# Kernel tuning notes

Measured on AMD Instinct MI355X. Metric: run time of the kernel, lower is better.

Reference implementation:

```python
import jax, jax.numpy as jnp
import numpy as np

B, D, O, E, H, K = 4096, 1024, 1024, 8, 4096, 2


def setup_inputs() -> dict:
    key = jax.random.key(0)
    ks = jax.random.split(key, 5)
    scale_g = 1.0 / np.sqrt(D)
    scale_1 = 1.0 / np.sqrt(D)
    scale_2 = 1.0 / np.sqrt(H)
    return {
        "x": jax.random.normal(ks[0], (B, D), jnp.float32),
        "gate_w": jax.random.normal(ks[1], (D, E), jnp.float32) * scale_g,
        "gate_b": jnp.zeros((E,), jnp.float32),
        "w1": jax.random.normal(ks[2], (E, D, H), jnp.float32) * scale_1,
        "b1": jnp.zeros((E, H), jnp.float32),
        "w2": jax.random.normal(ks[3], (E, H, O), jnp.float32) * scale_2,
        "b2": jnp.zeros((E, O), jnp.float32),
    }


def reference(x, gate_w, gate_b, w1, b1, w2, b2):
    # Router: top-k logits, softmax over the k selected logits only
    logits = x @ gate_w + gate_b                      # [B, E]
    top_vals, top_idx = jax.lax.top_k(logits, K)      # [B, K]
    routing_w = jax.nn.softmax(top_vals, axis=-1)     # [B, K]

    # Dense all-expert MLP (grouped GEMM), then gather the k selected outputs
    h = jax.nn.relu(jnp.einsum("bd,edh->beh", x, w1) + b1)  # [B, E, H]
    y = jnp.einsum("beh,eho->beo", h, w2) + b2              # [B, E, O]
    sel = jnp.take_along_axis(y, top_idx[:, :, None], axis=1)  # [B, K, O]
    return jnp.sum(routing_w[:, :, None] * sel, axis=1)        # [B, O]
```

## Files before the change

kernel.cpp:

```cpp
#include <hip/hip_runtime.h>
#include <stdint.h>

typedef short bf16x8 __attribute__((ext_vector_type(8)));
typedef float f32x4  __attribute__((ext_vector_type(4)));

constexpr int BT = 4096;
constexpr int DD = 1024;
constexpr int OO = 1024;
constexpr int EE = 8;
constexpr int HH = 4096;
constexpr int SLOTS = 2 * BT;

constexpr int BM = 256, BN = 256, BK = 32;
constexpr int RING = 4;
constexpr int A_USH = BM * BK;
constexpr int SLOT_USH = (BM + BN) * BK;
constexpr int MAXT = 40;

__device__ __forceinline__ unsigned short f2bf(float f) {
  unsigned u = __float_as_uint(f);
  u += 0x7fffu + ((u >> 16) & 1u);
  return (unsigned short)(u >> 16);
}

__device__ __forceinline__ void glds16(const unsigned short* g, unsigned short* l) {
  __builtin_amdgcn_global_load_lds(
      (const __attribute__((address_space(1))) void*)g,
      (__attribute__((address_space(3))) void*)l, 16, 0, 0);
}

__global__ __launch_bounds__(256) void router_k(const float* __restrict__ x,
                                                const float* __restrict__ gw,
                                                const float* __restrict__ gb,
                                                unsigned short* __restrict__ xb,
                                                int* __restrict__ cnt,
                                                int* __restrict__ list,
                                                float* __restrict__ rw) {
  int wave = threadIdx.x >> 6, lane = threadIdx.x & 63;
  int b = blockIdx.x * 4 + wave;
  const float* xrow = x + (size_t)b * DD;
  float acc[8];
#pragma unroll
  for (int e = 0; e < 8; ++e) acc[e] = 0.f;
#pragma unroll
  for (int i = 0; i < 4; ++i) {
    int d0 = i * 256 + lane * 4;
    float4 v = *(const float4*)&xrow[d0];
    unsigned lo = (unsigned)f2bf(v.x) | ((unsigned)f2bf(v.y) << 16);
    unsigned hi = (unsigned)f2bf(v.z) | ((unsigned)f2bf(v.w) << 16);
    *(uint2*)&xb[(size_t)b * DD + d0] = make_uint2(lo, hi);
    const float* g0 = &gw[(size_t)d0 * 8];
    float fv[4] = {v.x, v.y, v.z, v.w};
#pragma unroll
    for (int q = 0; q < 4; ++q) {
      float4 ga = *(const float4*)&g0[q * 8];
      float4 gc = *(const float4*)&g0[q * 8 + 4];
      acc[0] += fv[q] * ga.x; acc[1] += fv[q] * ga.y;
      acc[2] += fv[q] * ga.z; acc[3] += fv[q] * ga.w;
      acc[4] += fv[q] * gc.x; acc[5] += fv[q] * gc.y;
      acc[6] += fv[q] * gc.z; acc[7] += fv[q] * gc.w;
    }
  }
#pragma unroll
  for (int off = 32; off > 0; off >>= 1) {
#pragma unroll
    for (int e = 0; e < 8; ++e) acc[e] += __shfl_down(acc[e], off);
  }
  if (lane == 0) {
    float v[8];
#pragma unroll
    for (int e = 0; e < 8; ++e) v[e] = acc[e] + gb[e];
    int i0 = 0;
#pragma unroll
    for (int e = 1; e < 8; ++e) if (v[e] > v[i0]) i0 = e;
    int i1 = (i0 == 0) ? 1 : 0;
#pragma unroll
    for (int e = 0; e < 8; ++e) if (e != i0 && v[e] > v[i1]) i1 = e;
    float e1 = __expf(v[i1] - v[i0]);
    float inv = 1.0f / (1.0f + e1);
    int p0 = atomicAdd(&cnt[i0], 1);
    list[i0 * BT + p0] = 2 * b;     rw[2 * b]     = inv;
    int p1 = atomicAdd(&cnt[i1], 1);
    list[i1 * BT + p1] = 2 * b + 1; rw[2 * b + 1] = e1 * inv;
  }
}

__global__ void tilemap_k(const int* __restrict__ cnt, int* __restrict__ tmap,
                          int* __restrict__ ntiles) {
  if (threadIdx.x == 0 && blockIdx.x == 0) {
    int t = 0, basewalk = 0;
    for (int e = 0; e < EE; ++e) {
      int c = cnt[e];
      for (int m0 = 0; m0 < c; m0 += BM) {
        tmap[4 * t] = e; tmap[4 * t + 1] = m0; tmap[4 * t + 2] = basewalk + m0; ++t;
      }
      basewalk += c;
    }
    *ntiles = t;
  }
}

__global__ __launch_bounds__(256) void cvt_t_k(const float* __restrict__ src,
                                               unsigned short* __restrict__ dst,
                                               int R, int C) {
  __shared__ unsigned short tile[64][66];
  int e = blockIdx.z;
  const float* s = src + (size_t)e * R * C;
  unsigned short* d = dst + (size_t)e * R * C;
  int r0 = blockIdx.x << 6, c0 = blockIdx.y << 6;
  int t = threadIdx.x;
#pragma unroll
  for (int p = 0; p < 4; ++p) {
    int ch = p * 256 + t;
    int rr = ch >> 4, cc = (ch & 15) << 2;
    float4 v = *(const float4*)&s[(size_t)(r0 + rr) * C + c0 + cc];
    unsigned lo = (unsigned)f2bf(v.x) | ((unsigned)f2bf(v.y) << 16);
    unsigned hi = (unsigned)f2bf(v.z) | ((unsigned)f2bf(v.w) << 16);
    *(uint2*)&tile[rr][cc] = make_uint2(lo, hi);
  }
  __syncthreads();
#pragma unroll
  for (int p = 0; p < 4; ++p) {
    int ch = p * 256 + t;
    int cc = ch >> 4, rr = (ch & 15) << 2;
    unsigned short v0 = tile[rr + 0][cc];
    unsigned short v1 = tile[rr + 1][cc];
    unsigned short v2 = tile[rr + 2][cc];
    unsigned short v3 = tile[rr + 3][cc];
    unsigned lo = (unsigned)v0 | ((unsigned)v1 << 16);
    unsigned hi = (unsigned)v2 | ((unsigned)v3 << 16);
    *(uint2*)&d[(size_t)(c0 + cc) * R + r0 + rr] = make_uint2(lo, hi);
  }
}

__global__ __launch_bounds__(512, 2) void gemm1_k(const unsigned short* __restrict__ xb,
                                                  const unsigned short* __restrict__ w1t,
                                                  const float* __restrict__ b1,
                                                  const int* __restrict__ cnt,
                                                  const int* __restrict__ list,
                                                  const int* __restrict__ tmap,
                                                  const int* __restrict__ ntiles,
                                                  unsigned short* __restrict__ hc) {
  int ti = blockIdx.y;
  if (ti >= *ntiles) return;
  int e = tmap[4 * ti], m0 = tmap[4 * ti + 1], base = tmap[4 * ti + 2];
  int cnt_e = cnt[e];
  int n0 = blockIdx.x * BN;

  __shared__ int slotbuf[BM];
  __shared__ __align__(16) unsigned short lds[RING * SLOT_USH];

  int t = threadIdx.x;
  if (t < BM) {
    int r = m0 + t;
    slotbuf[t] = list[e * BT + (r < cnt_e ? r : 0)];
  }
  __syncthreads();

  int w = t >> 6, l = t & 63, lm = l & 15, lq = l >> 4;
  int wr = w >> 2, wc = w & 3;

  const unsigned short* aS[2];
  const unsigned short* bS[2];
  int dA[2], dB[2];
#pragma unroll
  for (int j = 0; j < 2; ++j) {
    int row = j * 128 + w * 16 + (l >> 2);
    int sch = ((l & 3) ^ ((row >> 1) & 3)) * 8;
    aS[j] = xb + (size_t)(slotbuf[row] >> 1) * DD + sch;
    bS[j] = w1t + (size_t)e * HH * DD + (size_t)(n0 + row) * DD + sch;
    dA[j] = j * 4096 + w * 512;
    dB[j] = A_USH + j * 4096 + w * 512;
  }

  int xc = lq ^ ((lm >> 1) & 3);
  int afo[8], bfo[4];
#pragma unroll
  for (int mi = 0; mi < 8; ++mi) afo[mi] = (wr * 128 + mi * 16 + lm) * BK + xc * 8;
#pragma unroll
  for (int ni = 0; ni < 4; ++ni) bfo[ni] = A_USH + (wc * 64 + ni * 16 + lm) * BK + xc * 8;

  f32x4 acc[8][4];
#pragma unroll
  for (int mi = 0; mi < 8; ++mi)
#pragma unroll
    for (int ni = 0; ni < 4; ++ni) acc[mi][ni] = f32x4{0.f, 0.f, 0.f, 0.f};

  constexpr int NT = DD / BK;

#pragma unroll
  for (int p = 0; p < RING - 1; ++p) {
    unsigned short* Lb = lds + p * SLOT_USH;
    glds16(aS[0] + p * BK, Lb + dA[0]);
    glds16(aS[1] + p * BK, Lb + dA[1]);
    glds16(bS[0] + p * BK, Lb + dB[0]);
    glds16(bS[1] + p * BK, Lb + dB[1]);
  }
  asm volatile("s_waitcnt vmcnt(8)" ::: "memory");
  __builtin_amdgcn_s_barrier();
  asm volatile("" ::: "memory");

  for (int tt = 0; tt < NT; ++tt) {
    {
      int ts = tt + 3;
      int ko = (ts < NT ? ts : NT - 1) * BK;
      unsigned short* Lb = lds + (ts & 3) * SLOT_USH;
      glds16(aS[0] + ko, Lb + dA[0]);
      glds16(aS[1] + ko, Lb + dA[1]);
      glds16(bS[0] + ko, Lb + dB[0]);
      glds16(bS[1] + ko, Lb + dB[1]);
    }
    const unsigned short* Lc = lds + (tt & 3) * SLOT_USH;
    bf16x8 af[8], bf[4];
#pragma unroll
    for (int mi = 0; mi < 8; ++mi) af[mi] = *(const bf16x8*)&Lc[afo[mi]];
#pragma unroll
    for (int ni = 0; ni < 4; ++ni) bf[ni] = *(const bf16x8*)&Lc[bfo[ni]];
    __builtin_amdgcn_s_setprio(1);
#pragma unroll
    for (int mi = 0; mi < 8; ++mi)
#pragma unroll
      for (int ni = 0; ni < 4; ++ni)
        acc[mi][ni] = __builtin_amdgcn_mfma_f32_16x16x32_bf16(af[mi], bf[ni], acc[mi][ni], 0, 0, 0);
    __builtin_amdgcn_s_setprio(0);
    asm volatile("s_waitcnt vmcnt(8)" ::: "memory");
    __builtin_amdgcn_s_barrier();
    asm volatile("" ::: "memory");
  }

  asm volatile("s_waitcnt vmcnt(0)" ::: "memory");
  __builtin_amdgcn_s_barrier();
  asm volatile("" ::: "memory");
  unsigned short* cb = lds + w * 8192;
  float bias[4];
#pragma unroll
  for (int ni = 0; ni < 4; ++ni) bias[ni] = b1[e * HH + n0 + wc * 64 + ni * 16 + lm];
#pragma unroll
  for (int mi = 0; mi < 8; ++mi)
#pragma unroll
    for (int ni = 0; ni < 4; ++ni)
#pragma unroll
      for (int r = 0; r < 4; ++r)
        cb[(mi * 16 + lq * 4 + r) * 64 + ni * 16 + lm] =
            f2bf(fmaxf(acc[mi][ni][r] + bias[ni], 0.0f));
  asm volatile("s_waitcnt lgkmcnt(0)" ::: "memory");
#pragma unroll
  for (int it = 0; it < 16; ++it) {
    int rr = it * 8 + (l >> 3), chk = l & 7;
    int grow = wr * 128 + rr;
    if (m0 + grow < cnt_e) {
      uint4 v = *(const uint4*)&cb[rr * 64 + chk * 8];
      *(uint4*)&hc[(size_t)(base + grow) * HH + n0 + wc * 64 + chk * 8] = v;
    }
  }
}

__global__ __launch_bounds__(512, 2) void gemm2_k(const unsigned short* __restrict__ hc,
                                                  const unsigned short* __restrict__ w2t,
                                                  const float* __restrict__ b2,
                                                  const int* __restrict__ cnt,
                                                  const int* __restrict__ list,
                                                  const int* __restrict__ tmap,
                                                  const int* __restrict__ ntiles,
                                                  const float* __restrict__ rw,
                                                  float* __restrict__ ybuf,
                                                  float* __restrict__ out) {
  int ti = blockIdx.y;
  if (ti >= *ntiles) return;
  int e = tmap[4 * ti], m0 = tmap[4 * ti + 1], base = tmap[4 * ti + 2];
  int cnt_e = cnt[e];
  int n0 = blockIdx.x * BN;
  int z = blockIdx.z;
  int ksl = HH / gridDim.z;
  int kb0 = z * ksl;
  int NT = ksl / BK;

  __shared__ int slotbuf[BM];
  __shared__ float rwbuf[BM];
  __shared__ __align__(16) unsigned short lds[RING * SLOT_USH];

  int t = threadIdx.x;
  if (t < BM) {
    int r = m0 + t;
    int s_ = list[e * BT + (r < cnt_e ? r : 0)];
    slotbuf[t] = s_;
    rwbuf[t] = rw[s_];
  }
  __syncthreads();

  int w = t >> 6, l = t & 63, lm = l & 15, lq = l >> 4;
  int wr = w >> 2, wc = w & 3;

  const unsigned short* aS[2];
  const unsigned short* bS[2];
  int dA[2], dB[2];
#pragma unroll
  for (int j = 0; j < 2; ++j) {
    int row = j * 128 + w * 16 + (l >> 2);
    int sch = ((l & 3) ^ ((row >> 1) & 3)) * 8;
    int gr = base + row; if (gr > SLOTS - 1) gr = SLOTS - 1;
    aS[j] = hc + (size_t)gr * HH + kb0 + sch;
    bS[j] = w2t + (size_t)e * OO * HH + (size_t)(n0 + row) * HH + kb0 + sch;
    dA[j] = j * 4096 + w * 512;
    dB[j] = A_USH + j * 4096 + w * 512;
  }

  int xc = lq ^ ((lm >> 1) & 3);
  int afo[8], bfo[4];
#pragma unroll
  for (int mi = 0; mi < 8; ++mi) afo[mi] = (wr * 128 + mi * 16 + lm) * BK + xc * 8;
#pragma unroll
  for (int ni = 0; ni < 4; ++ni) bfo[ni] = A_USH + (wc * 64 + ni * 16 + lm) * BK + xc * 8;

  f32x4 acc[8][4];
#pragma unroll
  for (int mi = 0; mi < 8; ++mi)
#pragma unroll
    for (int ni = 0; ni < 4; ++ni) acc[mi][ni] = f32x4{0.f, 0.f, 0.f, 0.f};

#pragma unroll
  for (int p = 0; p < RING - 1; ++p) {
    unsigned short* Lb = lds + p * SLOT_USH;
    glds16(aS[0] + p * BK, Lb + dA[0]);
    glds16(aS[1] + p * BK, Lb + dA[1]);
    glds16(bS[0] + p * BK, Lb + dB[0]);
    glds16(bS[1] + p * BK, Lb + dB[1]);
  }
  asm volatile("s_waitcnt vmcnt(8)" ::: "memory");
  __builtin_amdgcn_s_barrier();
  asm volatile("" ::: "memory");

  for (int tt = 0; tt < NT; ++tt) {
    {
      int ts = tt + 3;
      int ko = (ts < NT ? ts : NT - 1) * BK;
      unsigned short* Lb = lds + (ts & 3) * SLOT_USH;
      glds16(aS[0] + ko, Lb + dA[0]);
      glds16(aS[1] + ko, Lb + dA[1]);
      glds16(bS[0] + ko, Lb + dB[0]);
      glds16(bS[1] + ko, Lb + dB[1]);
    }
    const unsigned short* Lc = lds + (tt & 3) * SLOT_USH;
    bf16x8 af[8], bf[4];
#pragma unroll
    for (int mi = 0; mi < 8; ++mi) af[mi] = *(const bf16x8*)&Lc[afo[mi]];
#pragma unroll
    for (int ni = 0; ni < 4; ++ni) bf[ni] = *(const bf16x8*)&Lc[bfo[ni]];
    __builtin_amdgcn_s_setprio(1);
#pragma unroll
    for (int mi = 0; mi < 8; ++mi)
#pragma unroll
      for (int ni = 0; ni < 4; ++ni)
        acc[mi][ni] = __builtin_amdgcn_mfma_f32_16x16x32_bf16(af[mi], bf[ni], acc[mi][ni], 0, 0, 0);
    __builtin_amdgcn_s_setprio(0);
    asm volatile("s_waitcnt vmcnt(8)" ::: "memory");
    __builtin_amdgcn_s_barrier();
    asm volatile("" ::: "memory");
  }
  asm volatile("s_waitcnt vmcnt(0)" ::: "memory");

  bool addb = (z == 0);
  size_t ybase = (size_t)z * SLOTS;
#pragma unroll
  for (int ni = 0; ni < 4; ++ni) {
    int ncol = n0 + wc * 64 + ni * 16 + lm;
    float bias = addb ? b2[e * OO + ncol] : 0.0f;
#pragma unroll
    for (int mi = 0; mi < 8; ++mi)
#pragma unroll
      for (int r = 0; r < 4; ++r) {
        int lrow = wr * 128 + mi * 16 + lq * 4 + r;
        if (m0 + lrow < cnt_e) {
          float v = (acc[mi][ni][r] + bias) * rwbuf[lrow];
          int slot = slotbuf[lrow];
          if (ybuf) ybuf[(ybase + slot) * OO + ncol] = v;
          else      atomicAdd(&out[(size_t)(slot >> 1) * OO + ncol], v);
        }
      }
  }
}

__global__ __launch_bounds__(256) void combine_k(const float* __restrict__ y,
                                                 float* __restrict__ out, int nz) {
  int i = blockIdx.x * 256 + threadIdx.x;
  int b = i >> 8, c = i & 255;
  f32x4 acc = {0.f, 0.f, 0.f, 0.f};
  for (int z = 0; z < nz; ++z) {
#pragma unroll
    for (int k = 0; k < 2; ++k) {
      const float4 v = *(const float4*)&y[((size_t)z * SLOTS + 2 * b + k) * OO + c * 4];
      acc[0] += v.x; acc[1] += v.y; acc[2] += v.z; acc[3] += v.w;
    }
  }
  *(f32x4*)&out[(size_t)b * OO + c * 4] = acc;
}

extern "C" void kernel_launch(void* const* d_in, const int* in_sizes, int n_in,
                              void* d_out, int out_size, void* d_ws, size_t ws_size,
                              hipStream_t stream) {
  const float* x  = (const float*)d_in[0];
  const float* gw = (const float*)d_in[1];
  const float* gb = (const float*)d_in[2];
  const float* w1 = (const float*)d_in[3];
  const float* b1 = (const float*)d_in[4];
  const float* w2 = (const float*)d_in[5];
  const float* b2 = (const float*)d_in[6];
  float* out = (float*)d_out;
  char* ws = (char*)d_ws;

  int*            cnt    = (int*)(ws);
  int*            ntiles = (int*)(ws + 64);
  int*            tmap   = (int*)(ws + 128);
  float*          rw     = (float*)(ws + 4096);
  int*            list   = (int*)(ws + (64u << 10));
  unsigned short* xb     = (unsigned short*)(ws + (1u  << 20));
  unsigned short* wt     = (unsigned short*)(ws + (9u  << 20));
  unsigned short* hc     = (unsigned short*)(ws + (73u << 20));
  float*          ybuf   = (float*)(ws + (138u << 20));

  size_t need_min = (138u << 20);
  if (ws_size < need_min) return;
  int zsplit;
  float* ypass;
  if (ws_size >= (138u << 20) + (size_t)2 * SLOTS * OO * 4) { zsplit = 2; ypass = ybuf; }
  else if (ws_size >= (138u << 20) + (size_t)SLOTS * OO * 4) { zsplit = 1; ypass = ybuf; }
  else { zsplit = 2; ypass = nullptr; }

  hipMemsetAsync(cnt, 0, 64, stream);
  if (!ypass) hipMemsetAsync(out, 0, (size_t)BT * OO * sizeof(float), stream);

  router_k<<<BT / 4, 256, 0, stream>>>(x, gw, gb, xb, cnt, list, rw);
  tilemap_k<<<1, 64, 0, stream>>>(cnt, tmap, ntiles);
  cvt_t_k<<<dim3(DD / 64, HH / 64, EE), 256, 0, stream>>>(w1, wt, DD, HH);
  gemm1_k<<<dim3(HH / BN, MAXT), 512, 0, stream>>>(xb, wt, b1, cnt, list, tmap, ntiles, hc);
  cvt_t_k<<<dim3(HH / 64, OO / 64, EE), 256, 0, stream>>>(w2, wt, HH, OO);
  gemm2_k<<<dim3(OO / BN, MAXT, zsplit), 512, 0, stream>>>(hc, wt, b2, cnt, list, tmap, ntiles, rw, ypass, out);
  if (ypass)
    combine_k<<<BT * OO / 1024, 256, 0, stream>>>(ybuf, out, zsplit);
}
```

Before: 733.8 us.

## Shrink GEMM tiles to 128x128 and fuse weight conversion into router and GEMM1 launches

Both grouped GEMMs drop from 256x256 tiles with 512 threads and a 4-deep ring to 128x128 tiles with 256 threads, a 3-deep ring and 3 blocks per CU. MAXT rises to match the finer row tiling. The w1 transpose-convert is folded into the router launch as extra blocks, and when the workspace is large enough the w2 convert runs as extra blocks alongside GEMM1, writing to a separate buffer so the two can overlap. The aim is to cut launch count, fill CUs better with more, smaller blocks, and hide conversion work behind compute, at the cost of less operand reuse per tile and more redundant A/B traffic.

```diff
diff --git a/kernel.cpp b/kernel.cpp
--- a/kernel.cpp
+++ b/kernel.cpp
@@ -11,11 +11,11 @@
 constexpr int HH = 4096;
 constexpr int SLOTS = 2 * BT;
 
-constexpr int BM = 256, BN = 256, BK = 32;
-constexpr int RING = 4;
+constexpr int BM = 128, BN = 128, BK = 32;
 constexpr int A_USH = BM * BK;
 constexpr int SLOT_USH = (BM + BN) * BK;
-constexpr int MAXT = 40;
+constexpr int MAXT = 72;
+constexpr int G1_BLKS = 32 * MAXT;
 
 __device__ __forceinline__ unsigned short f2bf(float f) {
   unsigned u = __float_as_uint(f);
@@ -29,15 +29,56 @@
       (__attribute__((address_space(3))) void*)l, 16, 0, 0);
 }
 
-__global__ __launch_bounds__(256) void router_k(const float* __restrict__ x,
+__device__ __forceinline__ void cvt_body(const float* __restrict__ src,
+                                         unsigned short* __restrict__ dst,
+                                         int R, int C, int e, int r0, int c0, int t,
+                                         unsigned short (*tile)[66]) {
+  const float* s = src + (size_t)e * R * C;
+  unsigned short* d = dst + (size_t)e * R * C;
+#pragma unroll
+  for (int p = 0; p < 4; ++p) {
+    int ch = p * 256 + t;
+    int rr = ch >> 4, cc = (ch & 15) << 2;
+    float4 v = *(const float4*)&s[(size_t)(r0 + rr) * C + c0 + cc];
+    unsigned lo = (unsigned)f2bf(v.x) | ((unsigned)f2bf(v.y) << 16);
+    unsigned hi = (unsigned)f2bf(v.z) | ((unsigned)f2bf(v.w) << 16);
+    *(uint2*)&tile[rr][cc] = make_uint2(lo, hi);
+  }
+  __syncthreads();
+#pragma unroll
+  for (int p = 0; p < 4; ++p) {
+    int ch = p * 256 + t;
+    int cc = ch >> 4, rr = (ch & 15) << 2;
+    unsigned short v0 = tile[rr + 0][cc];
+    unsigned short v1 = tile[rr + 1][cc];
+    unsigned short v2 = tile[rr + 2][cc];
+    unsigned short v3 = tile[rr + 3][cc];
+    unsigned lo = (unsigned)v0 | ((unsigned)v1 << 16);
+    unsigned hi = (unsigned)v2 | ((unsigned)v3 << 16);
+    *(uint2*)&d[(size_t)(c0 + cc) * R + r0 + rr] = make_uint2(lo, hi);
+  }
+}
+
+__global__ __launch_bounds__(256) void fusedA_k(const float* __restrict__ x,
                                                 const float* __restrict__ gw,
                                                 const float* __restrict__ gb,
+                                                const float* __restrict__ w1,
                                                 unsigned short* __restrict__ xb,
                                                 int* __restrict__ cnt,
                                                 int* __restrict__ list,
-                                                float* __restrict__ rw) {
+                                                float* __restrict__ rw,
+                                                unsigned short* __restrict__ w1t) {
+  __shared__ unsigned short tile[64][66];
+  int bid = blockIdx.x;
+  if (bid >= 1024) {
+    int idx = bid - 1024;
+    int e = idx >> 10, rem = idx & 1023;
+    int r0 = (rem & 15) << 6, c0 = (rem >> 4) << 6;
+    cvt_body(w1, w1t, DD, HH, e, r0, c0, threadIdx.x, tile);
+    return;
+  }
   int wave = threadIdx.x >> 6, lane = threadIdx.x & 63;
-  int b = blockIdx.x * 4 + wave;
+  int b = bid * 4 + wave;
   const float* xrow = x + (size_t)b * DD;
   float acc[8];
 #pragma unroll
@@ -104,51 +145,36 @@
                                                unsigned short* __restrict__ dst,
                                                int R, int C) {
   __shared__ unsigned short tile[64][66];
-  int e = blockIdx.z;
-  const float* s = src + (size_t)e * R * C;
-  unsigned short* d = dst + (size_t)e * R * C;
-  int r0 = blockIdx.x << 6, c0 = blockIdx.y << 6;
-  int t = threadIdx.x;
-#pragma unroll
-  for (int p = 0; p < 4; ++p) {
-    int ch = p * 256 + t;
-    int rr = ch >> 4, cc = (ch & 15) << 2;
-    float4 v = *(const float4*)&s[(size_t)(r0 + rr) * C + c0 + cc];
-    unsigned lo = (unsigned)f2bf(v.x) | ((unsigned)f2bf(v.y) << 16);
-    unsigned hi = (unsigned)f2bf(v.z) | ((unsigned)f2bf(v.w) << 16);
-    *(uint2*)&tile[rr][cc] = make_uint2(lo, hi);
-  }
-  __syncthreads();
-#pragma unroll
-  for (int p = 0; p < 4; ++p) {
-    int ch = p * 256 + t;
-    int cc = ch >> 4, rr = (ch & 15) << 2;
-    unsigned short v0 = tile[rr + 0][cc];
-    unsigned short v1 = tile[rr + 1][cc];
-    unsigned short v2 = tile[rr + 2][cc];
-    unsigned short v3 = tile[rr + 3][cc];
-    unsigned lo = (unsigned)v0 | ((unsigned)v1 << 16);
-    unsigned hi = (unsigned)v2 | ((unsigned)v3 << 16);
-    *(uint2*)&d[(size_t)(c0 + cc) * R + r0 + rr] = make_uint2(lo, hi);
-  }
-}
-
-__global__ __launch_bounds__(512, 2) void gemm1_k(const unsigned short* __restrict__ xb,
-                                                  const unsigned short* __restrict__ w1t,
-                                                  const float* __restrict__ b1,
-                                                  const int* __restrict__ cnt,
-                                                  const int* __restrict__ list,
-                                                  const int* __restrict__ tmap,
-                                                  const int* __restrict__ ntiles,
-                                                  unsigned short* __restrict__ hc) {
-  int ti = blockIdx.y;
+  cvt_body(src, dst, R, C, blockIdx.z, blockIdx.x << 6, blockIdx.y << 6,
+           threadIdx.x, tile);
+}
+
+__global__ __launch_bounds__(256, 3) void fusedB_k(const unsigned short* __restrict__ xb,
+                                                   const unsigned short* __restrict__ w1t,
+                                                   const float* __restrict__ b1,
+                                                   const int* __restrict__ cnt,
+                                                   const int* __restrict__ list,
+                                                   const int* __restrict__ tmap,
+                                                   const int* __restrict__ ntiles,
+                                                   unsigned short* __restrict__ hc,
+                                                   const float* __restrict__ w2,
+                                                   unsigned short* __restrict__ w2t) {
+  __shared__ __align__(16) unsigned short lds[3 * SLOT_USH];
+  __shared__ int slotbuf[BM];
+  int bid = blockIdx.x;
+  if (bid >= G1_BLKS) {
+    int idx = bid - G1_BLKS;
+    int e = idx >> 10, rem = idx & 1023;
+    int r0 = (rem & 63) << 6, c0 = (rem >> 6) << 6;
+    cvt_body(w2, w2t, HH, OO, e, r0, c0, threadIdx.x,
+             (unsigned short (*)[66])lds);
+    return;
+  }
+  int ti = bid >> 5;
   if (ti >= *ntiles) return;
   int e = tmap[4 * ti], m0 = tmap[4 * ti + 1], base = tmap[4 * ti + 2];
   int cnt_e = cnt[e];
-  int n0 = blockIdx.x * BN;
-
-  __shared__ int slotbuf[BM];
-  __shared__ __align__(16) unsigned short lds[RING * SLOT_USH];
+  int n0 = (bid & 31) * BN;
 
   int t = threadIdx.x;
   if (t < BM) {
@@ -158,85 +184,88 @@
   __syncthreads();
 
   int w = t >> 6, l = t & 63, lm = l & 15, lq = l >> 4;
-  int wr = w >> 2, wc = w & 3;
+  int wm = (w >> 1) * 64, wn = (w & 1) * 64;
 
   const unsigned short* aS[2];
   const unsigned short* bS[2];
   int dA[2], dB[2];
 #pragma unroll
   for (int j = 0; j < 2; ++j) {
-    int row = j * 128 + w * 16 + (l >> 2);
+    int row = w * 32 + j * 16 + (l >> 2);
     int sch = ((l & 3) ^ ((row >> 1) & 3)) * 8;
     aS[j] = xb + (size_t)(slotbuf[row] >> 1) * DD + sch;
     bS[j] = w1t + (size_t)e * HH * DD + (size_t)(n0 + row) * DD + sch;
-    dA[j] = j * 4096 + w * 512;
-    dB[j] = A_USH + j * 4096 + w * 512;
-  }
-
-  int xc = lq ^ ((lm >> 1) & 3);
-  int afo[8], bfo[4];
-#pragma unroll
-  for (int mi = 0; mi < 8; ++mi) afo[mi] = (wr * 128 + mi * 16 + lm) * BK + xc * 8;
-#pragma unroll
-  for (int ni = 0; ni < 4; ++ni) bfo[ni] = A_USH + (wc * 64 + ni * 16 + lm) * BK + xc * 8;
-
-  f32x4 acc[8][4];
-#pragma unroll
-  for (int mi = 0; mi < 8; ++mi)
+    dA[j] = w * 1024 + j * 512;
+    dB[j] = A_USH + w * 1024 + j * 512;
+  }
+
+  int xs = (lq ^ ((lm >> 1) & 3)) * 8;
+  int afo[4], bfo[4];
+#pragma unroll
+  for (int mi = 0; mi < 4; ++mi) afo[mi] = (wm + mi * 16 + lm) * BK + xs;
+#pragma unroll
+  for (int ni = 0; ni < 4; ++ni) bfo[ni] = A_USH + (wn + ni * 16 + lm) * BK + xs;
+
+  f32x4 acc[4][4];
+#pragma unroll
+  for (int mi = 0; mi < 4; ++mi)
 #pragma unroll
     for (int ni = 0; ni < 4; ++ni) acc[mi][ni] = f32x4{0.f, 0.f, 0.f, 0.f};
 
   constexpr int NT = DD / BK;
 
 #pragma unroll
-  for (int p = 0; p < RING - 1; ++p) {
+  for (int p = 0; p < 2; ++p) {
     unsigned short* Lb = lds + p * SLOT_USH;
     glds16(aS[0] + p * BK, Lb + dA[0]);
     glds16(aS[1] + p * BK, Lb + dA[1]);
     glds16(bS[0] + p * BK, Lb + dB[0]);
     glds16(bS[1] + p * BK, Lb + dB[1]);
   }
-  asm volatile("s_waitcnt vmcnt(8)" ::: "memory");
+  asm volatile("s_waitcnt vmcnt(4)" ::: "memory");
   __builtin_amdgcn_s_barrier();
   asm volatile("" ::: "memory");
 
+  int sc = 0, ss = 2;
   for (int tt = 0; tt < NT; ++tt) {
     {
-      int ts = tt + 3;
+      int ts = tt + 2;
       int ko = (ts < NT ? ts : NT - 1) * BK;
-      unsigned short* Lb = lds + (ts & 3) * SLOT_USH;
+      unsigned short* Lb = lds + ss * SLOT_USH;
       glds16(aS[0] + ko, Lb + dA[0]);
       glds16(aS[1] + ko, Lb + dA[1]);
       glds16(bS[0] + ko, Lb + dB[0]);
       glds16(bS[1] + ko, Lb + dB[1]);
     }
-    const unsigned short* Lc = lds + (tt & 3) * SLOT_USH;
-    bf16x8 af[8], bf[4];
-#pragma unroll
-    for (int mi = 0; mi < 8; ++mi) af[mi] = *(const bf16x8*)&Lc[afo[mi]];
+    const unsigned short* Lc = lds + sc * SLOT_USH;
+    bf16x8 af[4], bf[4];
+#pragma unroll
+    for (int mi = 0; mi < 4; ++mi) af[mi] = *(const bf16x8*)&Lc[afo[mi]];
 #pragma unroll
     for (int ni = 0; ni < 4; ++ni) bf[ni] = *(const bf16x8*)&Lc[bfo[ni]];
     __builtin_amdgcn_s_setprio(1);
 #pragma unroll
-    for (int mi = 0; mi < 8; ++mi)
+    for (int mi = 0; mi < 4; ++mi)
 #pragma unroll
       for (int ni = 0; ni < 4; ++ni)
         acc[mi][ni] = __builtin_amdgcn_mfma_f32_16x16x32_bf16(af[mi], bf[ni], acc[mi][ni], 0, 0, 0);
     __builtin_amdgcn_s_setprio(0);
-    asm volatile("s_waitcnt vmcnt(8)" ::: "memory");
+    asm volatile("s_waitcnt vmcnt(4)" ::: "memory");
     __builtin_amdgcn_s_barrier();
     asm volatile("" ::: "memory");
+    if (++sc == 3) sc = 0;
+    if (++ss == 3) ss = 0;
   }
 
   asm volatile("s_waitcnt vmcnt(0)" ::: "memory");
   __builtin_amdgcn_s_barrier();
   asm volatile("" ::: "memory");
-  unsigned short* cb = lds + w * 8192;
+  unsigned short* cb = lds + w * 4096;
   float bias[4];
 #pragma unroll
-  for (int ni = 0; ni < 4; ++ni) bias[ni] = b1[e * HH + n0 + wc * 64 + ni * 16 + lm];
-#pragma unroll
-  for (int mi = 0; mi < 8; ++mi)
+  for (int ni = 0; ni < 4; ++ni) bias[ni] = b1[e * HH + n0 + wn + ni * 16 + lm];
+#pragma unroll
+  for (int mi = 0; mi < 4; ++mi)
 #pragma unroll
     for (int ni = 0; ni < 4; ++ni)
 #pragma unroll
@@ -245,17 +274,17 @@
             f2bf(fmaxf(acc[mi][ni][r] + bias[ni], 0.0f));
   asm volatile("s_waitcnt lgkmcnt(0)" ::: "memory");
 #pragma unroll
-  for (int it = 0; it < 16; ++it) {
+  for (int it = 0; it < 8; ++it) {
     int rr = it * 8 + (l >> 3), chk = l & 7;
-    int grow = wr * 128 + rr;
+    int grow = wm + rr;
     if (m0 + grow < cnt_e) {
       uint4 v = *(const uint4*)&cb[rr * 64 + chk * 8];
-      *(uint4*)&hc[(size_t)(base + grow) * HH + n0 + wc * 64 + chk * 8] = v;
-    }
-  }
-}
-
-__global__ __launch_bounds__(512, 2) void gemm2_k(const unsigned short* __restrict__ hc,
+      *(uint4*)&hc[(size_t)(base + grow) * HH + n0 + wn + chk * 8] = v;
+    }
+  }
+}
+
+__global__ __launch_bounds__(256, 3) void gemm2_k(const unsigned short* __restrict__ hc,
                                                   const unsigned short* __restrict__ w2t,
                                                   const float* __restrict__ b2,
                                                   const int* __restrict__ cnt,
@@ -271,13 +300,12 @@
   int cnt_e = cnt[e];
   int n0 = blockIdx.x * BN;
   int z = blockIdx.z;
-  int ksl = HH / gridDim.z;
-  int kb0 = z * ksl;
-  int NT = ksl / BK;
-
+  int kb0 = z * (HH / 2);
+  constexpr int NT = (HH / 2) / BK;
+
+  __shared__ __align__(16) unsigned short lds[3 * SLOT_USH];
   __shared__ int slotbuf[BM];
   __shared__ float rwbuf[BM];
-  __shared__ __align__(16) unsigned short lds[RING * SLOT_USH];
 
   int t = threadIdx.x;
   if (t < BM) {
@@ -289,73 +317,76 @@
   __syncthreads();
 
   int w = t >> 6, l = t & 63, lm = l & 15, lq = l >> 4;
-  int wr = w >> 2, wc = w & 3;
+  int wm = (w >> 1) * 64, wn = (w & 1) * 64;
 
   const unsigned short* aS[2];
   const unsigned short* bS[2];
   int dA[2], dB[2];
 #pragma unroll
   for (int j = 0; j < 2; ++j) {
-    int row = j * 128 + w * 16 + (l >> 2);
+    int row = w * 32 + j * 16 + (l >> 2);
     int sch = ((l & 3) ^ ((row >> 1) & 3)) * 8;
     int gr = base + row; if (gr > SLOTS - 1) gr = SLOTS - 1;
     aS[j] = hc + (size_t)gr * HH + kb0 + sch;
     bS[j] = w2t + (size_t)e * OO * HH + (size_t)(n0 + row) * HH + kb0 + sch;
-    dA[j] = j * 4096 + w * 512;
-    dB[j] = A_USH + j * 4096 + w * 512;
-  }
-
-  int xc = lq ^ ((lm >> 1) & 3);
-  int afo[8], bfo[4];
-#pragma unroll
-  for (int mi = 0; mi < 8; ++mi) afo[mi] = (wr * 128 + mi * 16 + lm) * BK + xc * 8;
-#pragma unroll
-  for (int ni = 0; ni < 4; ++ni) bfo[ni] = A_USH + (wc * 64 + ni * 16 + lm) * BK + xc * 8;
-
-  f32x4 acc[8][4];
-#pragma unroll
-  for (int mi = 0; mi < 8; ++mi)
+    dA[j] = w * 1024 + j * 512;
+    dB[j] = A_USH + w * 1024 + j * 512;
+  }
+
+  int xs = (lq ^ ((lm >> 1) & 3)) * 8;
+  int afo[4], bfo[4];
+#pragma unroll
+  for (int mi = 0; mi < 4; ++mi) afo[mi] = (wm + mi * 16 + lm) * BK + xs;
+#pragma unroll
+  for (int ni = 0; ni < 4; ++ni) bfo[ni] = A_USH + (wn + ni * 16 + lm) * BK + xs;
+
+  f32x4 acc[4][4];
+#pragma unroll
+  for (int mi = 0; mi < 4; ++mi)
 #pragma unroll
     for (int ni = 0; ni < 4; ++ni) acc[mi][ni] = f32x4{0.f, 0.f, 0.f, 0.f};
 
 #pragma unroll
-  for (int p = 0; p < RING - 1; ++p) {
+  for (int p = 0; p < 2; ++p) {
     unsigned short* Lb = lds + p * SLOT_USH;
     glds16(aS[0] + p * BK, Lb + dA[0]);
     glds16(aS[1] + p * BK, Lb + dA[1]);
     glds16(bS[0] + p * BK, Lb + dB[0]);
     glds16(bS[1] + p * BK, Lb + dB[1]);
   }
-  asm volatile("s_waitcnt vmcnt(8)" ::: "memory");
+  asm volatile("s_waitcnt vmcnt(4)" ::: "memory");
   __builtin_amdgcn_s_barrier();
   asm volatile("" ::: "memory");
 
+  int sc = 0, ss = 2;
   for (int tt = 0; tt < NT; ++tt) {
     {
-      int ts = tt + 3;
+      int ts = tt + 2;
       int ko = (ts < NT ? ts : NT - 1) * BK;
-      unsigned short* Lb = lds + (ts & 3) * SLOT_USH;
+      unsigned short* Lb = lds + ss * SLOT_USH;
       glds16(aS[0] + ko, Lb + dA[0]);
       glds16(aS[1] + ko, Lb + dA[1]);
       glds16(bS[0] + ko, Lb + dB[0]);
       glds16(bS[1] + ko, Lb + dB[1]);
     }
-    const unsigned short* Lc = lds + (tt & 3) * SLOT_USH;
-    bf16x8 af[8], bf[4];
-#pragma unroll
-    for (int mi = 0; mi < 8; ++mi) af[mi] = *(const bf16x8*)&Lc[afo[mi]];
+    const unsigned short* Lc = lds + sc * SLOT_USH;
+    bf16x8 af[4], bf[4];
+#pragma unroll
+    for (int mi = 0; mi < 4; ++mi) af[mi] = *(const bf16x8*)&Lc[afo[mi]];
 #pragma unroll
     for (int ni = 0; ni < 4; ++ni) bf[ni] = *(const bf16x8*)&Lc[bfo[ni]];
     __builtin_amdgcn_s_setprio(1);
 #pragma unroll
-    for (int mi = 0; mi < 8; ++mi)
+    for (int mi = 0; mi < 4; ++mi)
 #pragma unroll
       for (int ni = 0; ni < 4; ++ni)
         acc[mi][ni] = __builtin_amdgcn_mfma_f32_16x16x32_bf16(af[mi], bf[ni], acc[mi][ni], 0, 0, 0);
     __builtin_amdgcn_s_setprio(0);
-    asm volatile("s_waitcnt vmcnt(8)" ::: "memory");
+    asm volatile("s_waitcnt vmcnt(4)" ::: "memory");
     __builtin_amdgcn_s_barrier();
     asm volatile("" ::: "memory");
+    if (++sc == 3) sc = 0;
+    if (++ss == 3) ss = 0;
   }
   asm volatile("s_waitcnt vmcnt(0)" ::: "memory");
 
@@ -363,13 +394,13 @@
   size_t ybase = (size_t)z * SLOTS;
 #pragma unroll
   for (int ni = 0; ni < 4; ++ni) {
-    int ncol = n0 + wc * 64 + ni * 16 + lm;
+    int ncol = n0 + wn + ni * 16 + lm;
     float bias = addb ? b2[e * OO + ncol] : 0.0f;
 #pragma unroll
-    for (int mi = 0; mi < 8; ++mi)
+    for (int mi = 0; mi < 4; ++mi)
 #pragma unroll
       for (int r = 0; r < 4; ++r) {
-        int lrow = wr * 128 + mi * 16 + lq * 4 + r;
+        int lrow = wm + mi * 16 + lq * 4 + r;
         if (m0 + lrow < cnt_e) {
           float v = (acc[mi][ni][r] + bias) * rwbuf[lrow];
           int slot = slotbuf[lrow];
@@ -414,27 +445,34 @@
   float*          rw     = (float*)(ws + 4096);
   int*            list   = (int*)(ws + (64u << 10));
   unsigned short* xb     = (unsigned short*)(ws + (1u  << 20));
-  unsigned short* wt     = (unsigned short*)(ws + (9u  << 20));
-  unsigned short* hc     = (unsigned short*)(ws + (73u << 20));
-  float*          ybuf   = (float*)(ws + (138u << 20));
-
-  size_t need_min = (138u << 20);
-  if (ws_size < need_min) return;
-  int zsplit;
-  float* ypass;
-  if (ws_size >= (138u << 20) + (size_t)2 * SLOTS * OO * 4) { zsplit = 2; ypass = ybuf; }
-  else if (ws_size >= (138u << 20) + (size_t)SLOTS * OO * 4) { zsplit = 1; ypass = ybuf; }
-  else { zsplit = 2; ypass = nullptr; }
-
+  unsigned short* w1t    = (unsigned short*)(ws + (9u  << 20));
+
+  bool roomy = ws_size >= (201u << 20);
   hipMemsetAsync(cnt, 0, 64, stream);
-  if (!ypass) hipMemsetAsync(out, 0, (size_t)BT * OO * sizeof(float), stream);
-
-  router_k<<<BT / 4, 256, 0, stream>>>(x, gw, gb, xb, cnt, list, rw);
-  tilemap_k<<<1, 64, 0, stream>>>(cnt, tmap, ntiles);
-  cvt_t_k<<<dim3(DD / 64, HH / 64, EE), 256, 0, stream>>>(w1, wt, DD, HH);
-  gemm1_k<<<dim3(HH / BN, MAXT), 512, 0, stream>>>(xb, wt, b1, cnt, list, tmap, ntiles, hc);
-  cvt_t_k<<<dim3(HH / 64, OO / 64, EE), 256, 0, stream>>>(w2, wt, HH, OO);
-  gemm2_k<<<dim3(OO / BN, MAXT, zsplit), 512, 0, stream>>>(hc, wt, b2, cnt, list, tmap, ntiles, rw, ypass, out);
-  if (ypass)
-    combine_k<<<BT * OO / 1024, 256, 0, stream>>>(ybuf, out, zsplit);
-}
+
+  if (roomy) {
+    unsigned short* w2t = (unsigned short*)(ws + (73u  << 20));
+    unsigned short* hc  = (unsigned short*)(ws + (137u << 20));
+    float*          ybuf = (float*)(ws + (9u << 20));
+
+    fusedA_k<<<1024 + 8192, 256, 0, stream>>>(x, gw, gb, w1, xb, cnt, list, rw, w1t);
+    tilemap_k<<<1, 64, 0, stream>>>(cnt, tmap, ntiles);
+    fusedB_k<<<G1_BLKS + 8192, 256, 0, stream>>>(xb, w1t, b1, cnt, list, tmap, ntiles,
+                                                 hc, w2, w2t);
+    gemm2_k<<<dim3(OO / BN, MAXT, 2), 256, 0, stream>>>(hc, w2t, b2, cnt, list, tmap,
+                                                        ntiles, rw, ybuf, out);
+    combine_k<<<BT * OO / 1024, 256, 0, stream>>>(ybuf, out, 2);
+  } else {
+    if (ws_size < (137u << 20)) return;
+    unsigned short* w2t = w1t;
+    unsigned short* hc  = (unsigned short*)(ws + (73u << 20));
+    hipMemsetAsync(out, 0, (size_t)BT * OO * sizeof(float), stream);
+    fusedA_k<<<1024 + 8192, 256, 0, stream>>>(x, gw, gb, w1, xb, cnt, list, rw, w1t);
+    tilemap_k<<<1, 64, 0, stream>>>(cnt, tmap, ntiles);
+    fusedB_k<<<G1_BLKS, 256, 0, stream>>>(xb, w1t, b1, cnt, list, tmap, ntiles,
+                                          hc, w2, w2t);
+    cvt_t_k<<<dim3(HH / 64, OO / 64, EE), 256, 0, stream>>>(w2, w2t, HH, OO);
+    gemm2_k<<<dim3(OO / BN, MAXT, 2), 256, 0, stream>>>(hc, w2t, b2, cnt, list, tmap,
+                                                        ntiles, rw, nullptr, out);
+  }
+}
```

Measured after the change: 650.2 us. -11.4%, faster.
